# Performance work log

Measured on AMD Instinct MI355X. Metric: run time of the kernel, lower is better.

## Reference

```python
import jax, jax.numpy as jnp
import numpy as np

B, T, C = 2, 2048, 1024
NH, NKV, HD = 16, 4, 64
THETA = 10000.0


def setup_inputs() -> dict:
    key = jax.random.key(0)
    k1, k2, k3 = jax.random.split(key, 3)
    x = jax.random.normal(k1, (B, T, C), dtype=jnp.float32)
    W_qkv = jax.random.normal(k2, (C, (NH + 2 * NKV) * HD), dtype=jnp.float32) * 0.02
    W_proj = jax.random.normal(k3, (C, C), dtype=jnp.float32) * 0.02
    return {"x": x, "W_qkv": W_qkv, "W_proj": W_proj}


def _rope_tables(t_len):
    inv_freq = 1.0 / (THETA ** (jnp.arange(0, HD, 2, dtype=jnp.float32) / HD))  # [HD/2]
    t = jnp.arange(t_len, dtype=jnp.float32)
    freqs = jnp.outer(t, inv_freq)  # [T, HD/2]
    return jnp.cos(freqs), jnp.sin(freqs)


def _apply_rope(x, cos, sin):
    # x: [B, T, H, D] with interleaved pairs (even/odd lanes)
    x1 = x[..., 0::2]
    x2 = x[..., 1::2]
    cos = cos[None, :, None, :]
    sin = sin[None, :, None, :]
    o1 = x1 * cos - x2 * sin
    o2 = x1 * sin + x2 * cos
    return jnp.stack([o1, o2], axis=-1).reshape(x.shape)


def reference(x, W_qkv, W_proj):
    qkv = x @ W_qkv  # [B, T, (NH+2*NKV)*HD]
    q, k, v = jnp.split(qkv, [NH * HD, NH * HD + NKV * HD], axis=2)
    q = q.reshape(B, T, NH, HD)
    k = k.reshape(B, T, NKV, HD)
    v = v.reshape(B, T, NKV, HD)
    cos, sin = _rope_tables(T)
    q = _apply_rope(q, cos, sin)
    k = _apply_rope(k, cos, sin)
    rep = NH // NKV
    k = jnp.repeat(k, rep, axis=2)  # GQA: [B, T, NH, HD]
    v = jnp.repeat(v, rep, axis=2)
    att = jnp.einsum('bqhd,bkhd->bhqk', q, k) / jnp.sqrt(jnp.float32(HD))
    causal = jnp.tril(jnp.ones((T, T), dtype=bool))
    att = jnp.where(causal[None, None], att, -jnp.inf)
    att = jax.nn.softmax(att, axis=-1)
    y = jnp.einsum('bhqk,bkhd->bqhd', att, v).reshape(B, T, C)
    return y @ W_proj
```

## Files before the change

kernel.cpp:

```cpp
#include <hip/hip_runtime.h>
#include <hip/hip_bf16.h>

#define B_ 2
#define T_ 2048
#define C_ 1024
#define NH_ 16
#define NKV_ 4
#define HD_ 64
#define NQKV_ 1536
#define M_ 4096

typedef __attribute__((ext_vector_type(8))) __bf16 bf16x8;
typedef __attribute__((ext_vector_type(4))) __bf16 bf16x4;
typedef __attribute__((ext_vector_type(2))) __bf16 bf16x2;
typedef __attribute__((ext_vector_type(4))) float f32x4;
typedef __attribute__((ext_vector_type(4))) unsigned int u32x4;

__device__ __forceinline__ float fast_exp2(float x) { return __builtin_amdgcn_exp2f(x); }

#define GLOAD_LDS16(gptr, lptr)                                                        \
  __builtin_amdgcn_global_load_lds(                                                    \
      (const __attribute__((address_space(1))) unsigned int*)(gptr),                   \
      (__attribute__((address_space(3))) unsigned int*)(lptr), 16, 0, 0)

__device__ __forceinline__ void transpose_tile_body(const float* __restrict__ in,
                                                    __bf16* __restrict__ out,
                                                    int K, int N, int n0, int k0,
                                                    __bf16 (*tile)[72], int tid) {
  const int tr = tid >> 4, tc4 = (tid & 15) << 2;
  #pragma unroll
  for (int p = 0; p < 4; ++p) {
    const int k = k0 + p * 16 + tr;
    const float4 v = *(const float4*)&in[(size_t)k * N + n0 + tc4];
    tile[tc4 + 0][p * 16 + tr] = (__bf16)v.x;
    tile[tc4 + 1][p * 16 + tr] = (__bf16)v.y;
    tile[tc4 + 2][p * 16 + tr] = (__bf16)v.z;
    tile[tc4 + 3][p * 16 + tr] = (__bf16)v.w;
  }
  __syncthreads();
  #pragma unroll
  for (int p = 0; p < 4; ++p) {
    const int n = n0 + p * 16 + tr;
    bf16x4 o;
    o.x = tile[p * 16 + tr][tc4 + 0];
    o.y = tile[p * 16 + tr][tc4 + 1];
    o.z = tile[p * 16 + tr][tc4 + 2];
    o.w = tile[p * 16 + tr][tc4 + 3];
    *(bf16x4*)&out[(size_t)n * K + k0 + tc4] = o;
  }
}

#define NB_CASTX 2048
#define NB_TWQKV 384
#define NB_TWPROJ 256
#define PREP_GRID (NB_CASTX + NB_TWQKV + NB_TWPROJ + 256)
__global__ __launch_bounds__(256) void prep_kernel(const float* __restrict__ x,
                                                   const float* __restrict__ Wqkv,
                                                   const float* __restrict__ Wproj,
                                                   __bf16* __restrict__ xb,
                                                   __bf16* __restrict__ wqkvT,
                                                   __bf16* __restrict__ wprojT,
                                                   float* __restrict__ cosT,
                                                   float* __restrict__ sinT) {
  __shared__ __bf16 tile[64][72];
  const int blk = blockIdx.x, tid = threadIdx.x;
  if (blk < NB_CASTX) {
    const int i = blk * 256 + tid;
    const float4 v0 = ((const float4*)x)[2 * i];
    const float4 v1 = ((const float4*)x)[2 * i + 1];
    bf16x8 o;
    o[0] = (__bf16)v0.x; o[1] = (__bf16)v0.y; o[2] = (__bf16)v0.z; o[3] = (__bf16)v0.w;
    o[4] = (__bf16)v1.x; o[5] = (__bf16)v1.y; o[6] = (__bf16)v1.z; o[7] = (__bf16)v1.w;
    ((bf16x8*)xb)[i] = o;
  } else if (blk < NB_CASTX + NB_TWQKV) {
    const int bx = blk - NB_CASTX;
    transpose_tile_body(Wqkv, wqkvT, C_, NQKV_, (bx % (NQKV_ / 64)) * 64,
                        (bx / (NQKV_ / 64)) * 64, tile, tid);
  } else if (blk < NB_CASTX + NB_TWQKV + NB_TWPROJ) {
    const int bx = blk - NB_CASTX - NB_TWQKV;
    transpose_tile_body(Wproj, wprojT, C_, C_, (bx % (C_ / 64)) * 64,
                        (bx / (C_ / 64)) * 64, tile, tid);
  } else {
    const int idx = (blk - NB_CASTX - NB_TWQKV - NB_TWPROJ) * 256 + tid;
    const int t = idx >> 5, i = idx & 31;
    const float inv = powf(10000.0f, -(float)i * (1.0f / 32.0f));
    const float ang = (float)t * inv;
    cosT[idx] = cosf(ang);
    sinT[idx] = sinf(ang);
  }
}

template <typename OutT>
__global__ __launch_bounds__(256) void gemm_tn_kernel(const __bf16* __restrict__ A,
                                                      const __bf16* __restrict__ Bt,
                                                      OutT* __restrict__ C, int N, int K) {
  __shared__ __align__(16) __bf16 lA[2][128 * 64];
  __shared__ __align__(16) __bf16 lB[2][64 * 64];
  const int tid = threadIdx.x;
  const int lane = tid & 63;
  const int wave = tid >> 6;
  const int wr = wave >> 1, wc = wave & 1;
  const int m0 = blockIdx.y * 128, n0 = blockIdx.x * 64;
  const int srow = tid >> 3, kc = tid & 7;
  const int r16 = lane & 15, g = lane >> 4;
  f32x4 acc[4][2] = {};
  const int nt = K >> 6;

#define GSTAGE(buf, k0)                                                                   \
  {                                                                                       \
    _Pragma("unroll")                                                                     \
    for (int p = 0; p < 4; ++p) {                                                         \
      const int row = p * 32 + srow;                                                      \
      const int sw = (kc ^ (row & 7)) * 8;                                                \
      GLOAD_LDS16(&A[(size_t)(m0 + row) * K + (k0) + sw], &lA[buf][row * 64 + kc * 8]);   \
    }                                                                                     \
    _Pragma("unroll")                                                                     \
    for (int p = 0; p < 2; ++p) {                                                         \
      const int row = p * 32 + srow;                                                      \
      const int sw = (kc ^ (row & 7)) * 8;                                                \
      GLOAD_LDS16(&Bt[(size_t)(n0 + row) * K + (k0) + sw], &lB[buf][row * 64 + kc * 8]);  \
    }                                                                                     \
  }

  GSTAGE(0, 0);
  asm volatile("s_waitcnt vmcnt(0)" ::: "memory");
  __syncthreads();
  int cur = 0;
  for (int t = 0; t < nt; ++t) {
    if (t + 1 < nt) GSTAGE(cur ^ 1, (t + 1) << 6);
    #pragma unroll
    for (int ks = 0; ks < 64; ks += 32) {
      bf16x8 af[4], bfr[2];
      const int kch = (ks >> 3) + g;
      #pragma unroll
      for (int mi = 0; mi < 4; ++mi) {
        const int row = wr * 64 + mi * 16 + r16;
        af[mi] = *(const bf16x8*)&lA[cur][row * 64 + (kch ^ (row & 7)) * 8];
      }
      #pragma unroll
      for (int ni = 0; ni < 2; ++ni) {
        const int row = wc * 32 + ni * 16 + r16;
        bfr[ni] = *(const bf16x8*)&lB[cur][row * 64 + (kch ^ (row & 7)) * 8];
      }
      #pragma unroll
      for (int mi = 0; mi < 4; ++mi)
        #pragma unroll
        for (int ni = 0; ni < 2; ++ni)
          acc[mi][ni] = __builtin_amdgcn_mfma_f32_16x16x32_bf16(af[mi], bfr[ni], acc[mi][ni], 0, 0, 0);
    }
    asm volatile("s_waitcnt vmcnt(0)" ::: "memory");
    __syncthreads();
    cur ^= 1;
  }
  #pragma unroll
  for (int mi = 0; mi < 4; ++mi) {
    const int r0 = m0 + wr * 64 + mi * 16 + g * 4;
    #pragma unroll
    for (int ni = 0; ni < 2; ++ni) {
      const int c = n0 + wc * 32 + ni * 16 + r16;
      #pragma unroll
      for (int j = 0; j < 4; ++j)
        C[(size_t)(r0 + j) * N + c] = (OutT)acc[mi][ni][j];
    }
  }
#undef GSTAGE
}

#define NB_ROPEQK 2560
#define POST_GRID (NB_ROPEQK + 256)
__global__ __launch_bounds__(256) void post_kernel(const __bf16* __restrict__ qkv,
                                                   const float* __restrict__ cosT,
                                                   const float* __restrict__ sinT,
                                                   __bf16* __restrict__ Q,
                                                   __bf16* __restrict__ Kb,
                                                   __bf16* __restrict__ Vt) {
  __shared__ __bf16 tile[64][72];
  const int tid = threadIdx.x;
  if (blockIdx.x < NB_ROPEQK) {
    const int idx = blockIdx.x * 256 + tid;
    const int i8 = idx & 7;
    const int rest = idx >> 3;
    const int head = rest % (NH_ + NKV_);
    const int row = rest / (NH_ + NKV_);
    const int b = row >> 11, t = row & 2047;
    const float4 cv = *(const float4*)&cosT[t * 32 + i8 * 4];
    const float4 sv = *(const float4*)&sinT[t * 32 + i8 * 4];
    const bf16x8 v = *(const bf16x8*)&qkv[(size_t)row * NQKV_ + head * HD_ + i8 * 8];
    const bool isq = head < NH_;
    const float qs = isq ? 0.125f * 1.44269504f : 1.0f;
    bf16x8 o;
    #pragma unroll
    for (int p = 0; p < 4; ++p) {
      const float x1 = (float)v[2 * p], x2 = (float)v[2 * p + 1];
      const float c = (&cv.x)[p], s = (&sv.x)[p];
      o[2 * p]     = (__bf16)((x1 * c - x2 * s) * qs);
      o[2 * p + 1] = (__bf16)((x1 * s + x2 * c) * qs);
    }
    __bf16* dst = isq ? &Q[(((size_t)b * NH_ + head) * T_ + t) * HD_ + i8 * 8]
                      : &Kb[(((size_t)b * NKV_ + (head - NH_)) * T_ + t) * HD_ + i8 * 8];
    *(bf16x8*)dst = o;
  } else {
    const int blk = blockIdx.x - NB_ROPEQK;
    const int t0 = (blk & 31) * 64;
    const int kvh = (blk >> 5) & 3;
    const int b = blk >> 7;
    const int tr = tid >> 4, c4 = (tid & 15) << 2;
    #pragma unroll
    for (int p = 0; p < 4; ++p) {
      const int t = t0 + p * 16 + tr;
      const bf16x4 v = *(const bf16x4*)&qkv[(size_t)(b * T_ + t) * NQKV_ + (NH_ + NKV_) * HD_ + kvh * HD_ + c4];
      tile[c4 + 0][p * 16 + tr] = v.x;
      tile[c4 + 1][p * 16 + tr] = v.y;
      tile[c4 + 2][p * 16 + tr] = v.z;
      tile[c4 + 3][p * 16 + tr] = v.w;
    }
    __syncthreads();
    #pragma unroll
    for (int p = 0; p < 4; ++p) {
      const int d = p * 16 + tr;
      bf16x4 o;
      o.x = tile[d][c4 + 0]; o.y = tile[d][c4 + 1];
      o.z = tile[d][c4 + 2]; o.w = tile[d][c4 + 3];
      *(bf16x4*)&Vt[(((size_t)b * NKV_ + kvh) * HD_ + d) * T_ + t0 + c4] = o;
    }
  }
}

__global__ __launch_bounds__(256) void attn_kernel(const __bf16* __restrict__ Q,
                                                   const __bf16* __restrict__ Kb,
                                                   const __bf16* __restrict__ Vt,
                                                   __bf16* __restrict__ Y) {
  __shared__ __align__(16) __bf16 lK[2][64 * 64];
  __shared__ __align__(16) __bf16 lV[2][64 * 64];
  __shared__ __align__(16) __bf16 pP[4][16 * 64];
  const int tid = threadIdx.x;
  const int lane = tid & 63, wave = tid >> 6;
  const int r16 = lane & 15, g = lane >> 4;
  const int logical = (blockIdx.x & 7) * 64 + (blockIdx.x >> 3);
  const int i = logical & 15;
  const int bh = logical >> 4;
  const int b = bh >> 4, h = bh & 15;
  const int kvh = h >> 2;
  const __bf16* Qp = Q + ((size_t)b * NH_ + h) * T_ * HD_;
  const __bf16* Kp = Kb + ((size_t)b * NKV_ + kvh) * T_ * HD_;
  const __bf16* Vp = Vt + ((size_t)b * NKV_ + kvh) * HD_ * T_;
  const int qtile[2] = { i, 31 - i };
  const int srow = tid >> 3, kc = tid & 7;

#define ASTAGE(buf, kv0_)                                                                  \
  {                                                                                        \
    _Pragma("unroll")                                                                      \
    for (int p = 0; p < 2; ++p) {                                                          \
      const int row = p * 32 + srow;                                                       \
      const int sw = (kc ^ (row & 7)) * 8;                                                 \
      GLOAD_LDS16(&Kp[(size_t)((kv0_) + row) * HD_ + sw], &lK[buf][row * 64 + kc * 8]);    \
      GLOAD_LDS16(&Vp[(size_t)row * T_ + (kv0_) + sw], &lV[buf][row * 64 + kc * 8]);       \
    }                                                                                      \
  }

  bf16x8 qf[2][2];
  #pragma unroll
  for (int sd = 0; sd < 2; ++sd)
    #pragma unroll
    for (int c = 0; c < 2; ++c)
      qf[sd][c] = *(const bf16x8*)&Qp[(size_t)(qtile[sd] * 64 + wave * 16 + r16) * HD_ + (c * 4 + g) * 8];

  f32x4 o[2][4] = {};
  float mS[2], lS[2];
  #pragma unroll
  for (int sd = 0; sd < 2; ++sd) { mS[sd] = -__builtin_inff(); lS[sd] = 0.0f; }

  auto sm_side = [&](f32x4 (&s)[4], int sd) {
    float t0 = fmaxf(fmaxf(s[0][0], s[0][1]), s[0][2]);
    float t1 = fmaxf(fmaxf(s[0][3], s[1][0]), s[1][1]);
    float t2 = fmaxf(fmaxf(s[1][2], s[1][3]), s[2][0]);
    float t3 = fmaxf(fmaxf(s[2][1], s[2][2]), s[2][3]);
    float t4 = fmaxf(fmaxf(s[3][0], s[3][1]), s[3][2]);
    float pm = fmaxf(fmaxf(t0, t1), t2);
    pm = fmaxf(pm, fmaxf(t3, t4));
    pm = fmaxf(pm, s[3][3]);
    pm = fmaxf(pm, __shfl_xor(pm, 16));
    pm = fmaxf(pm, __shfl_xor(pm, 32));
    const bool upd = pm > mS[sd] + 8.0f;
    const float nm = upd ? pm : mS[sd];
    const float sc = fast_exp2(mS[sd] - nm);
    mS[sd] = nm;
    lS[sd] *= sc;
    if (__any(upd)) {
      #pragma unroll
      for (int j = 0; j < 4; ++j) {
        const float scj = __shfl(sc, g * 4 + j);
        #pragma unroll
        for (int nf = 0; nf < 4; ++nf) o[sd][nf][j] *= scj;
      }
    }
    float rs = 0.0f;
    #pragma unroll
    for (int ni = 0; ni < 4; ++ni) {
      bf16x4 pb;
      #pragma unroll
      for (int j = 0; j < 4; ++j) {
        const float pv = fast_exp2(s[ni][j] - mS[sd]);
        rs += pv;
        pb[j] = (__bf16)pv;
      }
      const int ch = 2 * ni + (g >> 1);
      *(bf16x4*)&pP[wave][r16 * 64 + ((ch ^ (r16 & 7)) * 8) + (g & 1) * 4] = pb;
    }
    rs += __shfl_xor(rs, 16);
    rs += __shfl_xor(rs, 32);
    lS[sd] += rs;
  };

  const int ntiles = 32 - i;
  ASTAGE(0, 0);
  asm volatile("s_waitcnt vmcnt(0)" ::: "memory");
  __syncthreads();
  int cur = 0;

  for (int t = 0; t < ntiles; ++t) {
    const int kv0 = t << 6;
    if (t + 1 < ntiles) ASTAGE(cur ^ 1, kv0 + 64);

    bf16x8 kf[2][4], vf[2][4];
    #pragma unroll
    for (int c = 0; c < 2; ++c)
      #pragma unroll
      for (int ni = 0; ni < 4; ++ni) {
        const int row = ni * 16 + r16;
        const int sw = ((c * 4 + g) ^ (row & 7)) * 8;
        kf[c][ni] = *(const bf16x8*)&lK[cur][row * 64 + sw];
        vf[c][ni] = *(const bf16x8*)&lV[cur][row * 64 + sw];
      }

    #pragma unroll
    for (int sd = 0; sd < 2; ++sd) {
      if (sd == 0 && t > i) continue;
      const int qw = qtile[sd] * 64 + wave * 16;

      f32x4 s[4] = {};
      #pragma unroll
      for (int c = 0; c < 2; ++c)
        #pragma unroll
        for (int ni = 0; ni < 4; ++ni)
          s[ni] = __builtin_amdgcn_mfma_f32_16x16x32_bf16(kf[c][ni], qf[sd][c], s[ni], 0, 0, 0);

      if (t == ((sd == 0) ? i : (ntiles - 1))) {
        #pragma unroll
        for (int ni = 0; ni < 4; ++ni)
          #pragma unroll
          for (int j = 0; j < 4; ++j)
            if (kv0 + ni * 16 + g * 4 + j > qw + r16) s[ni][j] = -__builtin_inff();
      }

      sm_side(s, sd);
      asm volatile("s_waitcnt lgkmcnt(0)" ::: "memory");

      #pragma unroll
      for (int c = 0; c < 2; ++c) {
        const bf16x8 pf = *(const bf16x8*)&pP[wave][r16 * 64 + (((c * 4 + g) ^ (r16 & 7)) * 8)];
        #pragma unroll
        for (int nf = 0; nf < 4; ++nf)
          o[sd][nf] = __builtin_amdgcn_mfma_f32_16x16x32_bf16(pf, vf[c][nf], o[sd][nf], 0, 0, 0);
      }
    }

    asm volatile("s_waitcnt vmcnt(0)" ::: "memory");
    __syncthreads();
    cur ^= 1;
  }

  #pragma unroll
  for (int sd = 0; sd < 2; ++sd) {
    const int qw = qtile[sd] * 64 + wave * 16;
    #pragma unroll
    for (int j = 0; j < 4; ++j) {
      const float lq = __shfl(lS[sd], g * 4 + j);
      const float inv = 1.0f / lq;
      const int tq = qw + g * 4 + j;
      #pragma unroll
      for (int nf = 0; nf < 4; ++nf) {
        const int d = nf * 16 + r16;
        Y[(((size_t)b * T_ + tq) * NH_ + h) * HD_ + d] = (__bf16)(o[sd][nf][j] * inv);
      }
    }
  }
#undef ASTAGE
}

extern "C" void kernel_launch(void* const* d_in, const int* in_sizes, int n_in,
                              void* d_out, int out_size, void* d_ws, size_t ws_size,
                              hipStream_t stream) {
  const float* x = (const float*)d_in[0];
  const float* Wqkv = (const float*)d_in[1];
  const float* Wproj = (const float*)d_in[2];
  float* out = (float*)d_out;

  char* ws = (char*)d_ws;
  size_t off = 0;
  auto alloc = [&](size_t bytes) {
    char* p = ws + off;
    off += (bytes + 255) & ~(size_t)255;
    return p;
  };
  __bf16* xb     = (__bf16*)alloc((size_t)M_ * C_ * 2);
  __bf16* wqkvT  = (__bf16*)alloc((size_t)NQKV_ * C_ * 2);
  __bf16* wprojT = (__bf16*)alloc((size_t)C_ * C_ * 2);
  float*  cosT   = (float*)alloc((size_t)T_ * 32 * 4);
  float*  sinT   = (float*)alloc((size_t)T_ * 32 * 4);
  __bf16* qkv    = (__bf16*)alloc((size_t)M_ * NQKV_ * 2);
  __bf16* Qb     = (__bf16*)alloc((size_t)B_ * NH_ * T_ * HD_ * 2);
  __bf16* Kb     = (__bf16*)alloc((size_t)B_ * NKV_ * T_ * HD_ * 2);
  __bf16* Vt     = (__bf16*)alloc((size_t)B_ * NKV_ * T_ * HD_ * 2);
  __bf16* Yb     = (__bf16*)alloc((size_t)M_ * C_ * 2);

  hipLaunchKernelGGL(prep_kernel, dim3(PREP_GRID), dim3(256), 0, stream,
                     x, Wqkv, Wproj, xb, wqkvT, wprojT, cosT, sinT);
  hipLaunchKernelGGL(HIP_KERNEL_NAME(gemm_tn_kernel<__bf16>), dim3(NQKV_ / 64, M_ / 128),
                     dim3(256), 0, stream, xb, wqkvT, qkv, NQKV_, C_);
  hipLaunchKernelGGL(post_kernel, dim3(POST_GRID), dim3(256), 0, stream,
                     qkv, cosT, sinT, Qb, Kb, Vt);
  hipLaunchKernelGGL(attn_kernel, dim3(16 * B_ * NH_), dim3(256), 0, stream, Qb, Kb, Vt, Yb);
  hipLaunchKernelGGL(HIP_KERNEL_NAME(gemm_tn_kernel<float>), dim3(C_ / 64, M_ / 128),
                     dim3(256), 0, stream, Yb, wprojT, out, C_, C_);
}
```

Before: 98.03 us.

## Fuse RoPE and V transpose into QKV GEMM epilogue; widen attention KV tile

The QKV GEMM epilogue now applies RoPE, the softmax scale and the head-major scatter directly, and writes V transposed. This removes the separate post kernel and the intermediate qkv buffer round trip. The attention kernel now processes 128 keys per tile instead of 64, halving the loop iterations and barriers. The cost is more LDS per block and scattered, uncoalesced scalar stores in the GEMM epilogue; K/V fragments are now read from LDS inside the MFMA loops instead of being preloaded.

```diff
diff --git a/kernel.cpp b/kernel.cpp
--- a/kernel.cpp
+++ b/kernel.cpp
@@ -12,7 +12,6 @@
 
 typedef __attribute__((ext_vector_type(8))) __bf16 bf16x8;
 typedef __attribute__((ext_vector_type(4))) __bf16 bf16x4;
-typedef __attribute__((ext_vector_type(2))) __bf16 bf16x2;
 typedef __attribute__((ext_vector_type(4))) float f32x4;
 typedef __attribute__((ext_vector_type(4))) unsigned int u32x4;
 
@@ -90,10 +89,14 @@
   }
 }
 
-template <typename OutT>
-__global__ __launch_bounds__(256) void gemm_tn_kernel(const __bf16* __restrict__ A,
-                                                      const __bf16* __restrict__ Bt,
-                                                      OutT* __restrict__ C, int N, int K) {
+__global__ __launch_bounds__(256) void gemm_qkv_kernel(const __bf16* __restrict__ A,
+                                                       const __bf16* __restrict__ Bt,
+                                                       const float* __restrict__ cosT,
+                                                       const float* __restrict__ sinT,
+                                                       __bf16* __restrict__ Q,
+                                                       __bf16* __restrict__ Kb,
+                                                       __bf16* __restrict__ Vt) {
+  const int N = NQKV_, K = C_;
   __shared__ __align__(16) __bf16 lA[2][128 * 64];
   __shared__ __align__(16) __bf16 lB[2][64 * 64];
   const int tid = threadIdx.x;
@@ -121,7 +124,6 @@
       GLOAD_LDS16(&Bt[(size_t)(n0 + row) * K + (k0) + sw], &lB[buf][row * 64 + kc * 8]);  \
     }                                                                                     \
   }
-
   GSTAGE(0, 0);
   asm volatile("s_waitcnt vmcnt(0)" ::: "memory");
   __syncthreads();
@@ -152,6 +154,105 @@
     __syncthreads();
     cur ^= 1;
   }
+#undef GSTAGE
+  const int bx = blockIdx.x;
+  const bool isV = bx >= 20;
+  const bool isQ = bx < 16;
+  const float qs = 0.125f * 1.44269504f;
+  const bool evenD = (r16 & 1) == 0;
+  #pragma unroll
+  for (int mi = 0; mi < 4; ++mi) {
+    const int t0g = m0 + wr * 64 + mi * 16 + g * 4;
+    const int b = t0g >> 11, tq0 = t0g & 2047;
+    #pragma unroll
+    for (int ni = 0; ni < 2; ++ni) {
+      const int d = wc * 32 + ni * 16 + r16;
+      if (isV) {
+        const int hv = bx - 20;
+        bf16x4 o4;
+        #pragma unroll
+        for (int j = 0; j < 4; ++j) o4[j] = (__bf16)acc[mi][ni][j];
+        *(bf16x4*)&Vt[(((size_t)b * NKV_ + hv) * HD_ + d) * T_ + tq0] = o4;
+      } else {
+        const int ir = d >> 1;
+        #pragma unroll
+        for (int j = 0; j < 4; ++j) {
+          const float val = acc[mi][ni][j];
+          const float oth = __shfl_xor(val, 1);
+          const float c = cosT[(tq0 + j) * 32 + ir];
+          const float s = sinT[(tq0 + j) * 32 + ir];
+          float o = evenD ? (val * c - oth * s) : (oth * s + val * c);
+          if (isQ) {
+            Q[(((size_t)b * NH_ + bx) * T_ + tq0 + j) * HD_ + d] = (__bf16)(o * qs);
+          } else {
+            Kb[(((size_t)b * NKV_ + (bx - 16)) * T_ + tq0 + j) * HD_ + d] = (__bf16)o;
+          }
+        }
+      }
+    }
+  }
+}
+
+__global__ __launch_bounds__(256) void gemm_tn_kernel(const __bf16* __restrict__ A,
+                                                      const __bf16* __restrict__ Bt,
+                                                      float* __restrict__ C, int N, int K) {
+  __shared__ __align__(16) __bf16 lA[2][128 * 64];
+  __shared__ __align__(16) __bf16 lB[2][64 * 64];
+  const int tid = threadIdx.x;
+  const int lane = tid & 63;
+  const int wave = tid >> 6;
+  const int wr = wave >> 1, wc = wave & 1;
+  const int m0 = blockIdx.y * 128, n0 = blockIdx.x * 64;
+  const int srow = tid >> 3, kc = tid & 7;
+  const int r16 = lane & 15, g = lane >> 4;
+  f32x4 acc[4][2] = {};
+  const int nt = K >> 6;
+
+#define GSTAGE(buf, k0)                                                                   \
+  {                                                                                       \
+    _Pragma("unroll")                                                                     \
+    for (int p = 0; p < 4; ++p) {                                                         \
+      const int row = p * 32 + srow;                                                      \
+      const int sw = (kc ^ (row & 7)) * 8;                                                \
+      GLOAD_LDS16(&A[(size_t)(m0 + row) * K + (k0) + sw], &lA[buf][row * 64 + kc * 8]);   \
+    }                                                                                     \
+    _Pragma("unroll")                                                                     \
+    for (int p = 0; p < 2; ++p) {                                                         \
+      const int row = p * 32 + srow;                                                      \
+      const int sw = (kc ^ (row & 7)) * 8;                                                \
+      GLOAD_LDS16(&Bt[(size_t)(n0 + row) * K + (k0) + sw], &lB[buf][row * 64 + kc * 8]);  \
+    }                                                                                     \
+  }
+  GSTAGE(0, 0);
+  asm volatile("s_waitcnt vmcnt(0)" ::: "memory");
+  __syncthreads();
+  int cur = 0;
+  for (int t = 0; t < nt; ++t) {
+    if (t + 1 < nt) GSTAGE(cur ^ 1, (t + 1) << 6);
+    #pragma unroll
+    for (int ks = 0; ks < 64; ks += 32) {
+      bf16x8 af[4], bfr[2];
+      const int kch = (ks >> 3) + g;
+      #pragma unroll
+      for (int mi = 0; mi < 4; ++mi) {
+        const int row = wr * 64 + mi * 16 + r16;
+        af[mi] = *(const bf16x8*)&lA[cur][row * 64 + (kch ^ (row & 7)) * 8];
+      }
+      #pragma unroll
+      for (int ni = 0; ni < 2; ++ni) {
+        const int row = wc * 32 + ni * 16 + r16;
+        bfr[ni] = *(const bf16x8*)&lB[cur][row * 64 + (kch ^ (row & 7)) * 8];
+      }
+      #pragma unroll
+      for (int mi = 0; mi < 4; ++mi)
+        #pragma unroll
+        for (int ni = 0; ni < 2; ++ni)
+          acc[mi][ni] = __builtin_amdgcn_mfma_f32_16x16x32_bf16(af[mi], bfr[ni], acc[mi][ni], 0, 0, 0);
+    }
+    asm volatile("s_waitcnt vmcnt(0)" ::: "memory");
+    __syncthreads();
+    cur ^= 1;
+  }
   #pragma unroll
   for (int mi = 0; mi < 4; ++mi) {
     const int r0 = m0 + wr * 64 + mi * 16 + g * 4;
@@ -160,79 +261,19 @@
       const int c = n0 + wc * 32 + ni * 16 + r16;
       #pragma unroll
       for (int j = 0; j < 4; ++j)
-        C[(size_t)(r0 + j) * N + c] = (OutT)acc[mi][ni][j];
+        C[(size_t)(r0 + j) * N + c] = acc[mi][ni][j];
     }
   }
 #undef GSTAGE
-}
-
-#define NB_ROPEQK 2560
-#define POST_GRID (NB_ROPEQK + 256)
-__global__ __launch_bounds__(256) void post_kernel(const __bf16* __restrict__ qkv,
-                                                   const float* __restrict__ cosT,
-                                                   const float* __restrict__ sinT,
-                                                   __bf16* __restrict__ Q,
-                                                   __bf16* __restrict__ Kb,
-                                                   __bf16* __restrict__ Vt) {
-  __shared__ __bf16 tile[64][72];
-  const int tid = threadIdx.x;
-  if (blockIdx.x < NB_ROPEQK) {
-    const int idx = blockIdx.x * 256 + tid;
-    const int i8 = idx & 7;
-    const int rest = idx >> 3;
-    const int head = rest % (NH_ + NKV_);
-    const int row = rest / (NH_ + NKV_);
-    const int b = row >> 11, t = row & 2047;
-    const float4 cv = *(const float4*)&cosT[t * 32 + i8 * 4];
-    const float4 sv = *(const float4*)&sinT[t * 32 + i8 * 4];
-    const bf16x8 v = *(const bf16x8*)&qkv[(size_t)row * NQKV_ + head * HD_ + i8 * 8];
-    const bool isq = head < NH_;
-    const float qs = isq ? 0.125f * 1.44269504f : 1.0f;
-    bf16x8 o;
-    #pragma unroll
-    for (int p = 0; p < 4; ++p) {
-      const float x1 = (float)v[2 * p], x2 = (float)v[2 * p + 1];
-      const float c = (&cv.x)[p], s = (&sv.x)[p];
-      o[2 * p]     = (__bf16)((x1 * c - x2 * s) * qs);
-      o[2 * p + 1] = (__bf16)((x1 * s + x2 * c) * qs);
-    }
-    __bf16* dst = isq ? &Q[(((size_t)b * NH_ + head) * T_ + t) * HD_ + i8 * 8]
-                      : &Kb[(((size_t)b * NKV_ + (head - NH_)) * T_ + t) * HD_ + i8 * 8];
-    *(bf16x8*)dst = o;
-  } else {
-    const int blk = blockIdx.x - NB_ROPEQK;
-    const int t0 = (blk & 31) * 64;
-    const int kvh = (blk >> 5) & 3;
-    const int b = blk >> 7;
-    const int tr = tid >> 4, c4 = (tid & 15) << 2;
-    #pragma unroll
-    for (int p = 0; p < 4; ++p) {
-      const int t = t0 + p * 16 + tr;
-      const bf16x4 v = *(const bf16x4*)&qkv[(size_t)(b * T_ + t) * NQKV_ + (NH_ + NKV_) * HD_ + kvh * HD_ + c4];
-      tile[c4 + 0][p * 16 + tr] = v.x;
-      tile[c4 + 1][p * 16 + tr] = v.y;
-      tile[c4 + 2][p * 16 + tr] = v.z;
-      tile[c4 + 3][p * 16 + tr] = v.w;
-    }
-    __syncthreads();
-    #pragma unroll
-    for (int p = 0; p < 4; ++p) {
-      const int d = p * 16 + tr;
-      bf16x4 o;
-      o.x = tile[d][c4 + 0]; o.y = tile[d][c4 + 1];
-      o.z = tile[d][c4 + 2]; o.w = tile[d][c4 + 3];
-      *(bf16x4*)&Vt[(((size_t)b * NKV_ + kvh) * HD_ + d) * T_ + t0 + c4] = o;
-    }
-  }
 }
 
 __global__ __launch_bounds__(256) void attn_kernel(const __bf16* __restrict__ Q,
                                                    const __bf16* __restrict__ Kb,
                                                    const __bf16* __restrict__ Vt,
                                                    __bf16* __restrict__ Y) {
-  __shared__ __align__(16) __bf16 lK[2][64 * 64];
-  __shared__ __align__(16) __bf16 lV[2][64 * 64];
-  __shared__ __align__(16) __bf16 pP[4][16 * 64];
+  __shared__ __align__(16) __bf16 lK[2][128 * 64];
+  __shared__ __align__(16) __bf16 lV[2][64 * 128];
+  __shared__ __align__(16) __bf16 pP[4][16 * 128];
   const int tid = threadIdx.x;
   const int lane = tid & 63, wave = tid >> 6;
   const int r16 = lane & 15, g = lane >> 4;
@@ -246,15 +287,21 @@
   const __bf16* Vp = Vt + ((size_t)b * NKV_ + kvh) * HD_ * T_;
   const int qtile[2] = { i, 31 - i };
   const int srow = tid >> 3, kc = tid & 7;
+  const int vrow = tid >> 4, vkc = tid & 15;
 
 #define ASTAGE(buf, kv0_)                                                                  \
   {                                                                                        \
     _Pragma("unroll")                                                                      \
-    for (int p = 0; p < 2; ++p) {                                                          \
+    for (int p = 0; p < 4; ++p) {                                                          \
       const int row = p * 32 + srow;                                                       \
       const int sw = (kc ^ (row & 7)) * 8;                                                 \
       GLOAD_LDS16(&Kp[(size_t)((kv0_) + row) * HD_ + sw], &lK[buf][row * 64 + kc * 8]);    \
-      GLOAD_LDS16(&Vp[(size_t)row * T_ + (kv0_) + sw], &lV[buf][row * 64 + kc * 8]);       \
+    }                                                                                      \
+    _Pragma("unroll")                                                                      \
+    for (int p = 0; p < 4; ++p) {                                                          \
+      const int d = p * 16 + vrow;                                                         \
+      const int ch = vkc ^ (d & 7);                                                        \
+      GLOAD_LDS16(&Vp[(size_t)d * T_ + (kv0_) + ch * 8], &lV[buf][d * 128 + vkc * 8]);     \
     }                                                                                      \
   }
 
@@ -270,15 +317,13 @@
   #pragma unroll
   for (int sd = 0; sd < 2; ++sd) { mS[sd] = -__builtin_inff(); lS[sd] = 0.0f; }
 
-  auto sm_side = [&](f32x4 (&s)[4], int sd) {
-    float t0 = fmaxf(fmaxf(s[0][0], s[0][1]), s[0][2]);
-    float t1 = fmaxf(fmaxf(s[0][3], s[1][0]), s[1][1]);
-    float t2 = fmaxf(fmaxf(s[1][2], s[1][3]), s[2][0]);
-    float t3 = fmaxf(fmaxf(s[2][1], s[2][2]), s[2][3]);
-    float t4 = fmaxf(fmaxf(s[3][0], s[3][1]), s[3][2]);
-    float pm = fmaxf(fmaxf(t0, t1), t2);
-    pm = fmaxf(pm, fmaxf(t3, t4));
-    pm = fmaxf(pm, s[3][3]);
+  auto sm_side = [&](f32x4 (&s)[8], int sd) {
+    f32x4 v4 = s[0];
+    #pragma unroll
+    for (int ni = 1; ni < 8; ++ni)
+      #pragma unroll
+      for (int j = 0; j < 4; ++j) v4[j] = fmaxf(v4[j], s[ni][j]);
+    float pm = fmaxf(fmaxf(v4[0], v4[1]), fmaxf(v4[2], v4[3]));
     pm = fmaxf(pm, __shfl_xor(pm, 16));
     pm = fmaxf(pm, __shfl_xor(pm, 32));
     const bool upd = pm > mS[sd] + 8.0f;
@@ -296,7 +341,7 @@
     }
     float rs = 0.0f;
     #pragma unroll
-    for (int ni = 0; ni < 4; ++ni) {
+    for (int ni = 0; ni < 8; ++ni) {
       bf16x4 pb;
       #pragma unroll
       for (int j = 0; j < 4; ++j) {
@@ -305,49 +350,42 @@
         pb[j] = (__bf16)pv;
       }
       const int ch = 2 * ni + (g >> 1);
-      *(bf16x4*)&pP[wave][r16 * 64 + ((ch ^ (r16 & 7)) * 8) + (g & 1) * 4] = pb;
+      *(bf16x4*)&pP[wave][r16 * 128 + ((ch ^ (r16 & 15)) * 8) + (g & 1) * 4] = pb;
     }
     rs += __shfl_xor(rs, 16);
     rs += __shfl_xor(rs, 32);
     lS[sd] += rs;
   };
 
-  const int ntiles = 32 - i;
+  const int ntiles = (33 - i) >> 1;
+  const int diagA = i >> 1;
   ASTAGE(0, 0);
   asm volatile("s_waitcnt vmcnt(0)" ::: "memory");
   __syncthreads();
   int cur = 0;
 
   for (int t = 0; t < ntiles; ++t) {
-    const int kv0 = t << 6;
-    if (t + 1 < ntiles) ASTAGE(cur ^ 1, kv0 + 64);
-
-    bf16x8 kf[2][4], vf[2][4];
-    #pragma unroll
-    for (int c = 0; c < 2; ++c)
-      #pragma unroll
-      for (int ni = 0; ni < 4; ++ni) {
-        const int row = ni * 16 + r16;
-        const int sw = ((c * 4 + g) ^ (row & 7)) * 8;
-        kf[c][ni] = *(const bf16x8*)&lK[cur][row * 64 + sw];
-        vf[c][ni] = *(const bf16x8*)&lV[cur][row * 64 + sw];
-      }
+    const int kv0 = t << 7;
+    if (t + 1 < ntiles) ASTAGE(cur ^ 1, kv0 + 128);
 
     #pragma unroll
     for (int sd = 0; sd < 2; ++sd) {
-      if (sd == 0 && t > i) continue;
+      if (sd == 0 && t > diagA) continue;
       const int qw = qtile[sd] * 64 + wave * 16;
 
-      f32x4 s[4] = {};
+      f32x4 s[8] = {};
       #pragma unroll
       for (int c = 0; c < 2; ++c)
         #pragma unroll
-        for (int ni = 0; ni < 4; ++ni)
-          s[ni] = __builtin_amdgcn_mfma_f32_16x16x32_bf16(kf[c][ni], qf[sd][c], s[ni], 0, 0, 0);
-
-      if (t == ((sd == 0) ? i : (ntiles - 1))) {
-        #pragma unroll
-        for (int ni = 0; ni < 4; ++ni)
+        for (int ni = 0; ni < 8; ++ni) {
+          const int row = ni * 16 + r16;
+          const bf16x8 kf = *(const bf16x8*)&lK[cur][row * 64 + ((c * 4 + g) ^ (row & 7)) * 8];
+          s[ni] = __builtin_amdgcn_mfma_f32_16x16x32_bf16(kf, qf[sd][c], s[ni], 0, 0, 0);
+        }
+
+      if (t == ((sd == 0) ? diagA : (ntiles - 1))) {
+        #pragma unroll
+        for (int ni = 0; ni < 8; ++ni)
           #pragma unroll
           for (int j = 0; j < 4; ++j)
             if (kv0 + ni * 16 + g * 4 + j > qw + r16) s[ni][j] = -__builtin_inff();
@@ -357,11 +395,14 @@
       asm volatile("s_waitcnt lgkmcnt(0)" ::: "memory");
 
       #pragma unroll
-      for (int c = 0; c < 2; ++c) {
-        const bf16x8 pf = *(const bf16x8*)&pP[wave][r16 * 64 + (((c * 4 + g) ^ (r16 & 7)) * 8)];
-        #pragma unroll
-        for (int nf = 0; nf < 4; ++nf)
-          o[sd][nf] = __builtin_amdgcn_mfma_f32_16x16x32_bf16(pf, vf[c][nf], o[sd][nf], 0, 0, 0);
+      for (int c = 0; c < 4; ++c) {
+        const bf16x8 pf = *(const bf16x8*)&pP[wave][r16 * 128 + (((c * 4 + g) ^ (r16 & 15)) * 8)];
+        #pragma unroll
+        for (int nf = 0; nf < 4; ++nf) {
+          const int row = nf * 16 + r16;
+          const bf16x8 vf = *(const bf16x8*)&lV[cur][row * 128 + ((c * 4 + g) ^ (row & 7)) * 8];
+          o[sd][nf] = __builtin_amdgcn_mfma_f32_16x16x32_bf16(pf, vf, o[sd][nf], 0, 0, 0);
+        }
       }
     }
 
@@ -408,7 +449,6 @@
   __bf16* wprojT = (__bf16*)alloc((size_t)C_ * C_ * 2);
   float*  cosT   = (float*)alloc((size_t)T_ * 32 * 4);
   float*  sinT   = (float*)alloc((size_t)T_ * 32 * 4);
-  __bf16* qkv    = (__bf16*)alloc((size_t)M_ * NQKV_ * 2);
   __bf16* Qb     = (__bf16*)alloc((size_t)B_ * NH_ * T_ * HD_ * 2);
   __bf16* Kb     = (__bf16*)alloc((size_t)B_ * NKV_ * T_ * HD_ * 2);
   __bf16* Vt     = (__bf16*)alloc((size_t)B_ * NKV_ * T_ * HD_ * 2);
@@ -416,11 +456,9 @@
 
   hipLaunchKernelGGL(prep_kernel, dim3(PREP_GRID), dim3(256), 0, stream,
                      x, Wqkv, Wproj, xb, wqkvT, wprojT, cosT, sinT);
-  hipLaunchKernelGGL(HIP_KERNEL_NAME(gemm_tn_kernel<__bf16>), dim3(NQKV_ / 64, M_ / 128),
-                     dim3(256), 0, stream, xb, wqkvT, qkv, NQKV_, C_);
-  hipLaunchKernelGGL(post_kernel, dim3(POST_GRID), dim3(256), 0, stream,
-                     qkv, cosT, sinT, Qb, Kb, Vt);
+  hipLaunchKernelGGL(gemm_qkv_kernel, dim3(NQKV_ / 64, M_ / 128), dim3(256), 0, stream,
+                     xb, wqkvT, cosT, sinT, Qb, Kb, Vt);
   hipLaunchKernelGGL(attn_kernel, dim3(16 * B_ * NH_), dim3(256), 0, stream, Qb, Kb, Vt, Yb);
-  hipLaunchKernelGGL(HIP_KERNEL_NAME(gemm_tn_kernel<float>), dim3(C_ / 64, M_ / 128),
-                     dim3(256), 0, stream, Yb, wprojT, out, C_, C_);
-}
+  hipLaunchKernelGGL(gemm_tn_kernel, dim3(C_ / 64, M_ / 128), dim3(256), 0, stream,
+                     Yb, wprojT, out, C_, C_);
+}
```

After: 111.9 us. 1.14x slower.
